# Kernel optimization log

Measured on AMD Instinct MI355X. Metric: run time of the kernel, lower is better.

## Reference

```python
import jax, jax.numpy as jnp
import numpy as np

B, N, DIM = 4, 16384, 512
HEADS, DHEAD = 8, 64
INNER = HEADS * DHEAD  # 512
ID_NUM = 128           # window size
EPS = 1e-5


def _ln(x, g, b):
    m = jnp.mean(x, axis=-1, keepdims=True)
    v = jnp.mean(jnp.square(x - m), axis=-1, keepdims=True)
    return (x - m) * jax.lax.rsqrt(v + EPS) * g + b


def setup_inputs() -> dict:
    key = jax.random.key(0)
    ks = jax.random.split(key, 10)
    s_in = 1.0 / np.sqrt(DIM)
    s_inner = 1.0 / np.sqrt(INNER)
    return {
        "x": jax.random.normal(ks[0], (B, N, DIM), jnp.float32),
        "y": jax.random.normal(ks[1], (B, N, DIM), jnp.float32),
        # torch Linear weights are [out, in]
        "Wq": jax.random.normal(ks[2], (INNER, DIM), jnp.float32) * s_in,
        "gq": jnp.ones((INNER,), jnp.float32),
        "bq": jnp.zeros((INNER,), jnp.float32),
        "Wk": jax.random.normal(ks[3], (INNER, DIM), jnp.float32) * s_in,
        "gk": jnp.ones((INNER,), jnp.float32),
        "bk": jnp.zeros((INNER,), jnp.float32),
        "Wv": jax.random.normal(ks[4], (INNER, DIM), jnp.float32) * s_in,
        "Wout": jax.random.normal(ks[5], (DIM, INNER), jnp.float32) * s_inner,
        "bout": jnp.zeros((DIM,), jnp.float32),
    }


def reference(x, y, Wq, gq, bq, Wk, gk, bk, Wv, Wout, bout):
    b, n, _ = y.shape
    w = n // ID_NUM
    scale = DHEAD ** -0.5

    q = _ln(y @ Wq.T, gq, bq)   # [b, n, inner]
    k = _ln(x @ Wk.T, gk, bk)
    v = x @ Wv.T

    # 'b (w n) (h d) -> (b w) h n d'
    def split(t):
        return t.reshape(b * w, ID_NUM, HEADS, DHEAD).transpose(0, 2, 1, 3)

    q, k, v = split(q), split(k), split(v)
    dots = jnp.einsum('bhid,bhjd->bhij', q, k) * scale  # [(b w), h, id, id]
    attn = jax.nn.softmax(dots, axis=-1)
    out = jnp.einsum('bhij,bhjd->bhid', attn, v)
    # '(b w) h n d -> b (w n) (h d)'
    out = out.transpose(0, 2, 1, 3).reshape(b, n, INNER)
    y_new = y + out @ Wout.T + bout
    return (y_new, attn)
```

## Files before the change

### kernel.cpp

```cpp
#include <hip/hip_runtime.h>


typedef __attribute__((ext_vector_type(8))) short short8;
typedef __attribute__((ext_vector_type(4))) float f32x4;
typedef __attribute__((ext_vector_type(4))) unsigned short us4;
typedef __attribute__((ext_vector_type(8))) unsigned short us8;
typedef __attribute__((ext_vector_type(4))) float fv4;

__device__ __forceinline__ unsigned short f2bf(float f) {
  unsigned u = __builtin_bit_cast(unsigned, f);
  u += 0x7fffu + ((u >> 16) & 1u);
  return (unsigned short)(u >> 16);
}
__device__ __forceinline__ float bf2f(unsigned short h) {
  unsigned u = ((unsigned)h) << 16;
  return __builtin_bit_cast(float, u);
}

__global__ __launch_bounds__(256) void cvt_kernel(const float* __restrict__ src,
                                                  unsigned short* __restrict__ dst,
                                                  int n4) {
  int i = blockIdx.x * 256 + threadIdx.x;
  if (i >= n4) return;
  fv4 f = *(const fv4*)(src + (size_t)i * 4);
  us4 o;
  o[0] = f2bf(f[0]); o[1] = f2bf(f[1]); o[2] = f2bf(f[2]); o[3] = f2bf(f[3]);
  *(us4*)(dst + (size_t)i * 4) = o;
}

template <int FINAL>
__global__ __launch_bounds__(256) void gemm_bt(const unsigned short* __restrict__ A,
                                               const unsigned short* __restrict__ Bw,
                                               unsigned short* __restrict__ Cb,
                                               float* __restrict__ Cf,
                                               const float* __restrict__ yres,
                                               const float* __restrict__ bias,
                                               int ldc) {
  __shared__ __align__(16) unsigned short As[128 * 32];
  __shared__ __align__(16) unsigned short Bs[128 * 32];
  const int tid = threadIdx.x;
  const int lane = tid & 63;
  const int wv = tid >> 6;
  const int quad = lane >> 4;
  const int l16 = lane & 15;
  const size_t m0 = (size_t)blockIdx.x * 128;
  const int n0 = blockIdx.y * 128;
  const int wm = (wv >> 1) * 64;
  const int wn = (wv & 1) * 64;

  f32x4 acc[4][4];
#pragma unroll
  for (int i = 0; i < 4; i++)
#pragma unroll
    for (int j = 0; j < 4; j++) acc[i][j] = (f32x4){0.f, 0.f, 0.f, 0.f};

  int ma[2], koff[2];
#pragma unroll
  for (int i = 0; i < 2; i++) {
    int c = i * 256 + tid;
    int m = c >> 2;
    int kc = (c & 3) ^ ((m >> 2) & 3);
    ma[i] = m;
    koff[i] = kc * 16;
  }
  const char* Ab = (const char*)A;
  const char* Bb = (const char*)Bw;
  char* AsB = (char*)As;
  char* BsB = (char*)Bs;

  for (int ks = 0; ks < 512; ks += 32) {
#pragma unroll
    for (int i = 0; i < 2; i++) {
      const char* ga = Ab + ((m0 + (size_t)ma[i]) << 10) + ks * 2 + koff[i];
      const char* gb = Bb + (((size_t)(n0 + ma[i])) << 10) + ks * 2 + koff[i];
      __builtin_amdgcn_global_load_lds(
          (const __attribute__((address_space(1))) unsigned int*)ga,
          (__attribute__((address_space(3))) unsigned int*)(AsB + i * 4096 + wv * 1024),
          16, 0, 0);
      __builtin_amdgcn_global_load_lds(
          (const __attribute__((address_space(1))) unsigned int*)gb,
          (__attribute__((address_space(3))) unsigned int*)(BsB + i * 4096 + wv * 1024),
          16, 0, 0);
    }
    __syncthreads();

    short8 af[4], bf[4];
#pragma unroll
    for (int t = 0; t < 4; t++) {
      int m = wm + t * 16 + l16;
      af[t] = *(const short8*)&As[m * 32 + ((quad ^ ((m >> 2) & 3)) * 8)];
      int n = wn + t * 16 + l16;
      bf[t] = *(const short8*)&Bs[n * 32 + ((quad ^ ((n >> 2) & 3)) * 8)];
    }
#pragma unroll
    for (int mt = 0; mt < 4; mt++)
#pragma unroll
      for (int nt = 0; nt < 4; nt++)
        acc[mt][nt] =
            __builtin_amdgcn_mfma_f32_16x16x32_bf16(bf[nt], af[mt], acc[mt][nt], 0, 0, 0);
    __syncthreads();
  }

#pragma unroll
  for (int mt = 0; mt < 4; mt++) {
    size_t m = m0 + wm + mt * 16 + l16;
#pragma unroll
    for (int nt = 0; nt < 4; nt++) {
      int n = n0 + wn + nt * 16 + quad * 4;
      size_t idx = m * (size_t)ldc + n;
      if (FINAL) {
        fv4 yv = *(const fv4*)(yres + idx);
        fv4 bv = *(const fv4*)(bias + n);
        fv4 o;
#pragma unroll
        for (int r = 0; r < 4; r++) o[r] = acc[mt][nt][r] + yv[r] + bv[r];
        *(fv4*)(Cf + idx) = o;
      } else {
        us4 o;
#pragma unroll
        for (int r = 0; r < 4; r++) o[r] = f2bf(acc[mt][nt][r]);
        *(us4*)(Cb + idx) = o;
      }
    }
  }
}

__global__ __launch_bounds__(256) void ln_rows(unsigned short* __restrict__ t,
                                               const float* __restrict__ g,
                                               const float* __restrict__ b,
                                               int ld) {
  size_t row = (size_t)blockIdx.x * 4 + (threadIdx.x >> 6);
  int lane = threadIdx.x & 63;
  unsigned short* p = t + row * (size_t)ld + lane * 8;
  us8 raw = *(const us8*)p;
  float v[8];
#pragma unroll
  for (int i = 0; i < 8; i++) v[i] = bf2f(raw[i]);
  float s = 0.f;
#pragma unroll
  for (int i = 0; i < 8; i++) s += v[i];
#pragma unroll
  for (int off = 32; off; off >>= 1) s += __shfl_xor(s, off);
  float mean = s * (1.0f / 512.0f);
  float qs = 0.f;
#pragma unroll
  for (int i = 0; i < 8; i++) {
    float d = v[i] - mean;
    qs += d * d;
  }
#pragma unroll
  for (int off = 32; off; off >>= 1) qs += __shfl_xor(qs, off);
  float rstd = rsqrtf(qs * (1.0f / 512.0f) + 1e-5f);
  const float* gp = g + lane * 8;
  const float* bp = b + lane * 8;
  us8 o;
#pragma unroll
  for (int i = 0; i < 8; i++) o[i] = f2bf((v[i] - mean) * rstd * gp[i] + bp[i]);
  *(us8*)p = o;
}

#define KVLD 1024

__global__ __launch_bounds__(256) void attn_kernel(const unsigned short* __restrict__ q,
                                                   const unsigned short* __restrict__ kmat,
                                                   const unsigned short* __restrict__ v,
                                                   float* __restrict__ attn_out,
                                                   unsigned short* __restrict__ ctx) {
  __shared__ __align__(16) unsigned short vT[64 * 128];
  __shared__ __align__(16) unsigned short Ps[128 * 128];
  const int h = blockIdx.x;
  const int bw = blockIdx.y;
  const int tb = bw * 128;
  const int tid = threadIdx.x;
  const int lane = tid & 63;
  const int wv = tid >> 6;
  const int quad = lane >> 4;
  const int l16 = lane & 15;
  const int hoff = h * 64;

#pragma unroll
  for (int it = 0; it < 8; it++) {
    int idx = (it * 256 + tid) * 4;
    int t = idx >> 6;
    int d = idx & 63;
    us4 val = *(const us4*)&v[(size_t)(tb + t) * KVLD + hoff + d];
#pragma unroll
    for (int j = 0; j < 4; j++) {
      int dd = d + j;
      int cp = (t >> 3) ^ (dd & 15);
      vT[dd * 128 + cp * 8 + (t & 7)] = val[j];
    }
  }

  f32x4 acc[2][8];
#pragma unroll
  for (int mi = 0; mi < 2; mi++)
#pragma unroll
    for (int ni = 0; ni < 8; ni++) acc[mi][ni] = (f32x4){0.f, 0.f, 0.f, 0.f};

  short8 aq[2][2];
#pragma unroll
  for (int mi = 0; mi < 2; mi++) {
    int tok = tb + wv * 32 + mi * 16 + l16;
#pragma unroll
    for (int kk = 0; kk < 2; kk++)
      aq[mi][kk] = *(const short8*)&q[(size_t)tok * 512 + hoff + kk * 32 + quad * 8];
  }
#pragma unroll
  for (int ni = 0; ni < 8; ni++) {
    int ktok = tb + ni * 16 + l16;
    short8 bk0 = *(const short8*)&kmat[(size_t)ktok * KVLD + hoff + quad * 8];
    short8 bk1 = *(const short8*)&kmat[(size_t)ktok * KVLD + hoff + 32 + quad * 8];
#pragma unroll
    for (int mi = 0; mi < 2; mi++) {
      acc[mi][ni] = __builtin_amdgcn_mfma_f32_16x16x32_bf16(bk0, aq[mi][0], acc[mi][ni], 0, 0, 0);
      acc[mi][ni] = __builtin_amdgcn_mfma_f32_16x16x32_bf16(bk1, aq[mi][1], acc[mi][ni], 0, 0, 0);
    }
  }

  size_t abase = ((size_t)(bw * 8 + h)) << 14;
#pragma unroll
  for (int mi = 0; mi < 2; mi++) {
    float mx = acc[mi][0][0];
#pragma unroll
    for (int ni = 0; ni < 8; ni++)
#pragma unroll
      for (int r = 0; r < 4; r++) mx = fmaxf(mx, acc[mi][ni][r]);
    mx = fmaxf(mx, __shfl_xor(mx, 16));
    mx = fmaxf(mx, __shfl_xor(mx, 32));
    float pv[8][4];
    float sum = 0.f;
#pragma unroll
    for (int ni = 0; ni < 8; ni++)
#pragma unroll
      for (int r = 0; r < 4; r++) {
        pv[ni][r] = __expf((acc[mi][ni][r] - mx) * 0.125f);
        sum += pv[ni][r];
      }
    sum += __shfl_xor(sum, 16);
    sum += __shfl_xor(sum, 32);
    float inv = 1.0f / sum;
    int i = wv * 32 + mi * 16 + l16;
    int cpx = (i & 15);
#pragma unroll
    for (int ni = 0; ni < 8; ni++) {
      int j0 = ni * 16 + quad * 4;
      fv4 pq;
      us4 pb;
#pragma unroll
      for (int r = 0; r < 4; r++) {
        float p = pv[ni][r] * inv;
        pq[r] = p;
        pb[r] = f2bf(p);
      }
      *(fv4*)&attn_out[abase + (size_t)i * 128 + j0] = pq;
      int cp = (j0 >> 3) ^ cpx;
      *(us4*)&Ps[i * 128 + cp * 8 + (quad & 1) * 4] = pb;
    }
  }
  __syncthreads();

  f32x4 o[2][4];
#pragma unroll
  for (int mi = 0; mi < 2; mi++)
#pragma unroll
    for (int nt = 0; nt < 4; nt++) o[mi][nt] = (f32x4){0.f, 0.f, 0.f, 0.f};

#pragma unroll
  for (int ks = 0; ks < 4; ks++) {
    short8 vfr[4];
#pragma unroll
    for (int nt = 0; nt < 4; nt++) {
      int d = nt * 16 + l16;
      int cp = (ks * 4 + quad) ^ (d & 15);
      vfr[nt] = *(const short8*)&vT[d * 128 + cp * 8];
    }
#pragma unroll
    for (int mi = 0; mi < 2; mi++) {
      int i = wv * 32 + mi * 16 + l16;
      int cp = (ks * 4 + quad) ^ (i & 15);
      short8 pfr = *(const short8*)&Ps[i * 128 + cp * 8];
#pragma unroll
      for (int nt = 0; nt < 4; nt++)
        o[mi][nt] = __builtin_amdgcn_mfma_f32_16x16x32_bf16(vfr[nt], pfr, o[mi][nt], 0, 0, 0);
    }
  }
#pragma unroll
  for (int mi = 0; mi < 2; mi++) {
    int tok = tb + wv * 32 + mi * 16 + l16;
#pragma unroll
    for (int nt = 0; nt < 4; nt++) {
      int d0 = nt * 16 + quad * 4;
      us4 ov;
#pragma unroll
      for (int r = 0; r < 4; r++) ov[r] = f2bf(o[mi][nt][r]);
      *(us4*)&ctx[(size_t)tok * 512 + hoff + d0] = ov;
    }
  }
}

extern "C" void kernel_launch(void* const* d_in, const int* in_sizes, int n_in,
                              void* d_out, int out_size, void* d_ws, size_t ws_size,
                              hipStream_t stream) {
  const float* x = (const float*)d_in[0];
  const float* y = (const float*)d_in[1];
  const float* Wq = (const float*)d_in[2];
  const float* gq = (const float*)d_in[3];
  const float* bq = (const float*)d_in[4];
  const float* Wk = (const float*)d_in[5];
  const float* gk = (const float*)d_in[6];
  const float* bk = (const float*)d_in[7];
  const float* Wv = (const float*)d_in[8];
  const float* Wout = (const float*)d_in[9];
  const float* bout = (const float*)d_in[10];
  float* out = (float*)d_out;

  char* ws = (char*)d_ws;
  const size_t W = 524288;
  const size_t T = 67108864;
  unsigned short* WQB = (unsigned short*)(ws);
  unsigned short* WKVB = (unsigned short*)(ws + W);
  unsigned short* WOB = (unsigned short*)(ws + 3 * W);
  unsigned short* XB = (unsigned short*)(ws + 4 * W);
  unsigned short* YB = (unsigned short*)(ws + 4 * W + T);
  unsigned short* Q = (unsigned short*)(ws + 4 * W + 2 * T);
  unsigned short* KV = (unsigned short*)(ws + 4 * W + 3 * T);
  unsigned short* CTX = YB;

  cvt_kernel<<<256, 256, 0, stream>>>(Wq, WQB, 65536);
  cvt_kernel<<<256, 256, 0, stream>>>(Wk, WKVB, 65536);
  cvt_kernel<<<256, 256, 0, stream>>>(Wv, WKVB + 262144, 65536);
  cvt_kernel<<<256, 256, 0, stream>>>(Wout, WOB, 65536);
  cvt_kernel<<<32768, 256, 0, stream>>>(x, XB, 8388608);
  cvt_kernel<<<32768, 256, 0, stream>>>(y, YB, 8388608);

  gemm_bt<0><<<dim3(512, 4), 256, 0, stream>>>(YB, WQB, Q, nullptr, nullptr, nullptr, 512);
  gemm_bt<0><<<dim3(512, 8), 256, 0, stream>>>(XB, WKVB, KV, nullptr, nullptr, nullptr, 1024);

  ln_rows<<<16384, 256, 0, stream>>>(Q, gq, bq, 512);
  ln_rows<<<16384, 256, 0, stream>>>(KV, gk, bk, 1024);

  attn_kernel<<<dim3(8, 512), 256, 0, stream>>>(Q, KV, KV + 512, out + 33554432, CTX);

  gemm_bt<1><<<dim3(512, 4), 256, 0, stream>>>(CTX, WOB, nullptr, out, y, bout, 512);
}
```

Measured before the change: 1.023 ms.

## Fuse LayerNorm stats into projection GEMM epilogue and apply LN inside attention

The separate ln_rows passes over Q and K are removed. The projection GEMMs now emit per-row partial sums and sums of squares, a small kernel reduces these to mean and rstd, and the attention kernel normalizes Q and K on load. The change also merges the four weight conversions into one launch and remaps block IDs in the GEMMs and attention for XCD-aware locality. The goal is to avoid a full read-modify-write of the Q and K tensors. The cost is that variance is computed as E[x^2]-mean^2 from fp32 accumulators, and the output buffer is used as scratch space for the statistics.

```diff
diff --git a/kernel.cpp b/kernel.cpp
--- a/kernel.cpp
+++ b/kernel.cpp
@@ -6,6 +6,7 @@
 typedef __attribute__((ext_vector_type(4))) unsigned short us4;
 typedef __attribute__((ext_vector_type(8))) unsigned short us8;
 typedef __attribute__((ext_vector_type(4))) float fv4;
+typedef __attribute__((ext_vector_type(2))) float fv2;
 
 __device__ __forceinline__ unsigned short f2bf(float f) {
   unsigned u = __builtin_bit_cast(unsigned, f);
@@ -28,14 +29,38 @@
   *(us4*)(dst + (size_t)i * 4) = o;
 }
 
-template <int FINAL>
+__global__ __launch_bounds__(256) void cvt4_kernel(const float* __restrict__ s0,
+                                                   const float* __restrict__ s1,
+                                                   const float* __restrict__ s2,
+                                                   const float* __restrict__ s3,
+                                                   unsigned short* __restrict__ d0,
+                                                   unsigned short* __restrict__ d1,
+                                                   unsigned short* __restrict__ d2,
+                                                   unsigned short* __restrict__ d3) {
+  const float* s;
+  unsigned short* d;
+  switch (blockIdx.y) {
+    case 0: s = s0; d = d0; break;
+    case 1: s = s1; d = d1; break;
+    case 2: s = s2; d = d2; break;
+    default: s = s3; d = d3; break;
+  }
+  int i = blockIdx.x * 256 + threadIdx.x;
+  fv4 f = *(const fv4*)(s + (size_t)i * 4);
+  us4 o;
+  o[0] = f2bf(f[0]); o[1] = f2bf(f[1]); o[2] = f2bf(f[2]); o[3] = f2bf(f[3]);
+  *(us4*)(d + (size_t)i * 4) = o;
+}
+
+template <int FINAL, int LNS>
 __global__ __launch_bounds__(256) void gemm_bt(const unsigned short* __restrict__ A,
                                                const unsigned short* __restrict__ Bw,
                                                unsigned short* __restrict__ Cb,
                                                float* __restrict__ Cf,
                                                const float* __restrict__ yres,
                                                const float* __restrict__ bias,
-                                               int ldc) {
+                                               int ldc,
+                                               fv2* __restrict__ pstat) {
   __shared__ __align__(16) unsigned short As[128 * 32];
   __shared__ __align__(16) unsigned short Bs[128 * 32];
   const int tid = threadIdx.x;
@@ -43,8 +68,15 @@
   const int wv = tid >> 6;
   const int quad = lane >> 4;
   const int l16 = lane & 15;
-  const size_t m0 = (size_t)blockIdx.x * 128;
-  const int n0 = blockIdx.y * 128;
+
+  const int gy = gridDim.y;
+  const int sh = (gy == 8) ? 3 : 2;
+  const int nwg = (int)gridDim.x << sh;
+  const int hwid = blockIdx.y * gridDim.x + blockIdx.x;
+  const int w = (hwid & 7) * (nwg >> 3) + (hwid >> 3);
+  const size_t m0 = (size_t)(w >> sh) * 128;
+  const int n0 = (w & (gy - 1)) * 128;
+
   const int wm = (wv >> 1) * 64;
   const int wn = (wv & 1) * 64;
 
@@ -123,40 +155,54 @@
       }
     }
   }
-}
-
-__global__ __launch_bounds__(256) void ln_rows(unsigned short* __restrict__ t,
-                                               const float* __restrict__ g,
-                                               const float* __restrict__ b,
-                                               int ld) {
-  size_t row = (size_t)blockIdx.x * 4 + (threadIdx.x >> 6);
-  int lane = threadIdx.x & 63;
-  unsigned short* p = t + row * (size_t)ld + lane * 8;
-  us8 raw = *(const us8*)p;
-  float v[8];
-#pragma unroll
-  for (int i = 0; i < 8; i++) v[i] = bf2f(raw[i]);
-  float s = 0.f;
-#pragma unroll
-  for (int i = 0; i < 8; i++) s += v[i];
-#pragma unroll
-  for (int off = 32; off; off >>= 1) s += __shfl_xor(s, off);
+
+  if (LNS && n0 < 512) {
+#pragma unroll
+    for (int mt = 0; mt < 4; mt++) {
+      float s = 0.f, s2 = 0.f;
+#pragma unroll
+      for (int nt = 0; nt < 4; nt++)
+#pragma unroll
+        for (int r = 0; r < 4; r++) {
+          float t = acc[mt][nt][r];
+          s += t;
+          s2 += t * t;
+        }
+      s += __shfl_xor(s, 16);
+      s += __shfl_xor(s, 32);
+      s2 += __shfl_xor(s2, 16);
+      s2 += __shfl_xor(s2, 32);
+      if (quad == 0) {
+        size_t row = m0 + wm + mt * 16 + l16;
+        fv2 p;
+        p[0] = s;
+        p[1] = s2;
+        pstat[row * 8 + (n0 >> 7) * 2 + (wv & 1)] = p;
+      }
+    }
+  }
+}
+
+__global__ __launch_bounds__(256) void stats_fin(const fv2* __restrict__ pq,
+                                                 const fv2* __restrict__ pk,
+                                                 fv2* __restrict__ sq,
+                                                 fv2* __restrict__ sk) {
+  int row = blockIdx.x * 256 + threadIdx.x;
+  const fv2* p = blockIdx.y ? pk : pq;
+  fv2* so = blockIdx.y ? sk : sq;
+  float s = 0.f, s2 = 0.f;
+#pragma unroll
+  for (int i = 0; i < 8; i++) {
+    fv2 v = p[(size_t)row * 8 + i];
+    s += v[0];
+    s2 += v[1];
+  }
   float mean = s * (1.0f / 512.0f);
-  float qs = 0.f;
-#pragma unroll
-  for (int i = 0; i < 8; i++) {
-    float d = v[i] - mean;
-    qs += d * d;
-  }
-#pragma unroll
-  for (int off = 32; off; off >>= 1) qs += __shfl_xor(qs, off);
-  float rstd = rsqrtf(qs * (1.0f / 512.0f) + 1e-5f);
-  const float* gp = g + lane * 8;
-  const float* bp = b + lane * 8;
-  us8 o;
-#pragma unroll
-  for (int i = 0; i < 8; i++) o[i] = f2bf((v[i] - mean) * rstd * gp[i] + bp[i]);
-  *(us8*)p = o;
+  float var = s2 * (1.0f / 512.0f) - mean * mean;
+  fv2 o;
+  o[0] = mean;
+  o[1] = rsqrtf(var + 1e-5f);
+  so[row] = o;
 }
 
 #define KVLD 1024
@@ -164,12 +210,20 @@
 __global__ __launch_bounds__(256) void attn_kernel(const unsigned short* __restrict__ q,
                                                    const unsigned short* __restrict__ kmat,
                                                    const unsigned short* __restrict__ v,
+                                                   const fv2* __restrict__ sq,
+                                                   const fv2* __restrict__ sk,
+                                                   const float* __restrict__ gq,
+                                                   const float* __restrict__ bq,
+                                                   const float* __restrict__ gk,
+                                                   const float* __restrict__ bk,
                                                    float* __restrict__ attn_out,
                                                    unsigned short* __restrict__ ctx) {
   __shared__ __align__(16) unsigned short vT[64 * 128];
   __shared__ __align__(16) unsigned short Ps[128 * 128];
-  const int h = blockIdx.x;
-  const int bw = blockIdx.y;
+  const int hwid = blockIdx.x;
+  const int wk = (hwid & 7) * 512 + (hwid >> 3);
+  const int h = wk & 7;
+  const int bw = wk >> 3;
   const int tb = bw * 128;
   const int tid = threadIdx.x;
   const int lane = tid & 63;
@@ -202,15 +256,37 @@
 #pragma unroll
   for (int mi = 0; mi < 2; mi++) {
     int tok = tb + wv * 32 + mi * 16 + l16;
-#pragma unroll
-    for (int kk = 0; kk < 2; kk++)
-      aq[mi][kk] = *(const short8*)&q[(size_t)tok * 512 + hoff + kk * 32 + quad * 8];
+    fv2 st = sq[tok];
+#pragma unroll
+    for (int kk = 0; kk < 2; kk++) {
+      const float* gp = gq + hoff + kk * 32 + quad * 8;
+      const float* bp = bq + hoff + kk * 32 + quad * 8;
+      us8 raw = *(const us8*)&q[(size_t)tok * 512 + hoff + kk * 32 + quad * 8];
+      us8 o;
+#pragma unroll
+      for (int e = 0; e < 8; e++) {
+        float f = (bf2f(raw[e]) - st[0]) * st[1] * gp[e] + bp[e];
+        o[e] = f2bf(f);
+      }
+      aq[mi][kk] = __builtin_bit_cast(short8, o);
+    }
   }
 #pragma unroll
   for (int ni = 0; ni < 8; ni++) {
     int ktok = tb + ni * 16 + l16;
-    short8 bk0 = *(const short8*)&kmat[(size_t)ktok * KVLD + hoff + quad * 8];
-    short8 bk1 = *(const short8*)&kmat[(size_t)ktok * KVLD + hoff + 32 + quad * 8];
+    fv2 stk = sk[ktok];
+    us8 r0 = *(const us8*)&kmat[(size_t)ktok * KVLD + hoff + quad * 8];
+    us8 r1 = *(const us8*)&kmat[(size_t)ktok * KVLD + hoff + 32 + quad * 8];
+    const float* g0 = gk + hoff + quad * 8;
+    const float* b0 = bk + hoff + quad * 8;
+    us8 o0, o1;
+#pragma unroll
+    for (int e = 0; e < 8; e++) {
+      o0[e] = f2bf((bf2f(r0[e]) - stk[0]) * stk[1] * g0[e] + b0[e]);
+      o1[e] = f2bf((bf2f(r1[e]) - stk[0]) * stk[1] * g0[32 + e] + b0[32 + e]);
+    }
+    short8 bk0 = __builtin_bit_cast(short8, o0);
+    short8 bk1 = __builtin_bit_cast(short8, o1);
 #pragma unroll
     for (int mi = 0; mi < 2; mi++) {
       acc[mi][ni] = __builtin_amdgcn_mfma_f32_16x16x32_bf16(bk0, aq[mi][0], acc[mi][ni], 0, 0, 0);
@@ -327,20 +403,26 @@
   unsigned short* KV = (unsigned short*)(ws + 4 * W + 3 * T);
   unsigned short* CTX = YB;
 
-  cvt_kernel<<<256, 256, 0, stream>>>(Wq, WQB, 65536);
-  cvt_kernel<<<256, 256, 0, stream>>>(Wk, WKVB, 65536);
-  cvt_kernel<<<256, 256, 0, stream>>>(Wv, WKVB + 262144, 65536);
-  cvt_kernel<<<256, 256, 0, stream>>>(Wout, WOB, 65536);
+  fv2* Pq = (fv2*)(out);
+  fv2* Pk = (fv2*)(out + 2097152);
+  fv2* Sq = (fv2*)(out + 4194304);
+  fv2* Sk = (fv2*)(out + 6291456);
+
+  cvt4_kernel<<<dim3(256, 4), 256, 0, stream>>>(Wq, Wk, Wv, Wout, WQB, WKVB,
+                                                WKVB + 262144, WOB);
   cvt_kernel<<<32768, 256, 0, stream>>>(x, XB, 8388608);
   cvt_kernel<<<32768, 256, 0, stream>>>(y, YB, 8388608);
 
-  gemm_bt<0><<<dim3(512, 4), 256, 0, stream>>>(YB, WQB, Q, nullptr, nullptr, nullptr, 512);
-  gemm_bt<0><<<dim3(512, 8), 256, 0, stream>>>(XB, WKVB, KV, nullptr, nullptr, nullptr, 1024);
-
-  ln_rows<<<16384, 256, 0, stream>>>(Q, gq, bq, 512);
-  ln_rows<<<16384, 256, 0, stream>>>(KV, gk, bk, 1024);
-
-  attn_kernel<<<dim3(8, 512), 256, 0, stream>>>(Q, KV, KV + 512, out + 33554432, CTX);
-
-  gemm_bt<1><<<dim3(512, 4), 256, 0, stream>>>(CTX, WOB, nullptr, out, y, bout, 512);
-}
+  gemm_bt<0, 1><<<dim3(512, 4), 256, 0, stream>>>(YB, WQB, Q, nullptr, nullptr,
+                                                  nullptr, 512, Pq);
+  gemm_bt<0, 1><<<dim3(512, 8), 256, 0, stream>>>(XB, WKVB, KV, nullptr, nullptr,
+                                                  nullptr, 1024, Pk);
+
+  stats_fin<<<dim3(256, 2), 256, 0, stream>>>(Pq, Pk, Sq, Sk);
+
+  attn_kernel<<<4096, 256, 0, stream>>>(Q, KV, KV + 512, Sq, Sk, gq, bq, gk, bk,
+                                        out + 33554432, CTX);
+
+  gemm_bt<1, 0><<<dim3(512, 4), 256, 0, stream>>>(CTX, WOB, nullptr, out, y, bout,
+                                                  512, nullptr);
+}
```

Result: no change. 1.020 ms (-0.3%).
